# Kernel tuning notes

Hardware: AMD Instinct MI355X
Metric: run time of the kernel (lower is better)

Reference implementation:

```python
import jax, jax.numpy as jnp
import numpy as np
import math

B, S, D, H = 2, 2048, 1024, 16
DK = D // H
EPS = 1e-5

def setup_inputs() -> dict:
    key = jax.random.key(0)
    ks = jax.random.split(key, 16)
    s = 0.02
    return {
        'query': jax.random.normal(ks[0], (B, S, D), jnp.float32),
        'key': jax.random.normal(ks[1], (B, S, D), jnp.float32),
        'value': jax.random.normal(ks[2], (B, S, D), jnp.float32),
        'mask': jax.random.randint(ks[3], (B, 1, S, S), 0, 2, jnp.int32),
        'market_context': jax.random.normal(ks[4], (B, D), jnp.float32),
        'Wq': jax.random.normal(ks[5], (D, D), jnp.float32) * s,
        'bq': jnp.zeros((D,), jnp.float32),
        'Wk': jax.random.normal(ks[6], (D, D), jnp.float32) * s,
        'bk': jnp.zeros((D,), jnp.float32),
        'Wv': jax.random.normal(ks[7], (D, D), jnp.float32) * s,
        'bv': jnp.zeros((D,), jnp.float32),
        'Wo': jax.random.normal(ks[8], (D, D), jnp.float32) * s,
        'bo': jnp.zeros((D,), jnp.float32),
        'Wc': jax.random.normal(ks[9], (D, D), jnp.float32) * s,
        'bc': jnp.zeros((D,), jnp.float32),
        'ln_g': jnp.ones((D,), jnp.float32),
        'ln_b': jnp.zeros((D,), jnp.float32),
    }

def reference(query, key, value, mask, market_context,
              Wq, bq, Wk, bk, Wv, bv, Wo, bo, Wc, bc, ln_g, ln_b):
    b, s, d = query.shape
    # QKV projections -> [B, H, S, DK]
    Q = (query @ Wq + bq).reshape(b, s, H, DK).transpose(0, 2, 1, 3)
    K = (key @ Wk + bk).reshape(b, s, H, DK).transpose(0, 2, 1, 3)
    V = (value @ Wv + bv).reshape(b, s, H, DK).transpose(0, 2, 1, 3)
    # market context -> per-head bias added to K (broadcast over sequence)
    ctx = (market_context @ Wc + bc).reshape(b, H, DK)
    K = K + ctx[:, :, None, :]
    scores = jnp.einsum('bhqd,bhkd->bhqk', Q, K) / math.sqrt(DK)
    scores = jnp.where(mask == 0, jnp.float32(-1e9), scores)
    attn = jax.nn.softmax(scores, axis=-1)  # dropout is identity in eval
    ctx2 = jnp.einsum('bhqk,bhkd->bhqd', attn, V)
    ctx2 = ctx2.transpose(0, 2, 1, 3).reshape(b, s, d)
    out = ctx2 @ Wo + bo
    x = out + query
    mu = jnp.mean(x, axis=-1, keepdims=True)
    var = jnp.mean((x - mu) ** 2, axis=-1, keepdims=True)
    return (x - mu) * jax.lax.rsqrt(var + EPS) * ln_g + ln_b
```

## Files before the change

### kernel.cpp

```cpp
#include <hip/hip_runtime.h>
#include <cstdint>

typedef unsigned short u16;
typedef __attribute__((ext_vector_type(8))) short s16x8;
typedef __attribute__((ext_vector_type(8))) unsigned short u16x8;
typedef __attribute__((ext_vector_type(4))) float f32x4;
typedef __attribute__((ext_vector_type(16))) float f32x16;
typedef __attribute__((ext_vector_type(2))) unsigned uint2v;
typedef __attribute__((ext_vector_type(4))) unsigned uint4v;

#define CKF 0.18033688011f

__device__ inline u16 f2bf(float f){
  union { float f; uint32_t u; } v; v.f = f;
  uint32_t r = v.u + 0x7fffu + ((v.u >> 16) & 1u);
  return (u16)(r >> 16);
}

__device__ inline f32x4 mfma16(s16x8 a, s16x8 b, f32x4 c){
  return __builtin_amdgcn_mfma_f32_16x16x32_bf16(a, b, c, 0, 0, 0);
}
__device__ inline f32x16 mfma32(s16x8 a, s16x8 b, f32x16 c){
  return __builtin_amdgcn_mfma_f32_32x32x16_bf16(a, b, c, 0, 0, 0);
}
__device__ inline unsigned cvtpk(float a, float b){
  unsigned r;
  asm("v_cvt_pk_bf16_f32 %0, %1, %2" : "=v"(r) : "v"(a), "v"(b));
  return r;
}
__device__ inline float exp2a(float x){
  float r;
  asm("v_exp_f32 %0, %1" : "=v"(r) : "v"(x));
  return r;
}
__device__ inline void glds16(const u16* g, u16* l){
  __builtin_amdgcn_global_load_lds((const __attribute__((address_space(1))) void*)g,
                                   (__attribute__((address_space(3))) void*)l, 16, 0, 0);
}
__device__ inline void glds4(const unsigned* g, unsigned* l){
  __builtin_amdgcn_global_load_lds((const __attribute__((address_space(1))) void*)g,
                                   (__attribute__((address_space(3))) void*)l, 4, 0, 0);
}

struct PrepParams {
  const float* q; const float* k; const float* v;
  const int* mask; const float* mc;
  const float* W0; const float* W1; const float* W2; const float* W3;
  const float* Wc;
  u16* qo; u16* ko; u16* vo;
  u16* T0; u16* T1; u16* T2; u16* T3;
  unsigned* bits; float* part;
};

__global__ __launch_bounds__(256) void prep_kernel(PrepParams PP){
  __shared__ float shf[1056];
  int blk = blockIdx.x, tid = threadIdx.x;
  if (blk < 6144){
    int byy = blk >> 11, bxx = blk & 2047;
    const float* src = (byy == 0) ? PP.q : (byy == 1) ? PP.k : PP.v;
    u16* dst = (byy == 0) ? PP.qo : (byy == 1) ? PP.ko : PP.vo;
    size_t i = ((size_t)bxx * 256 + tid) * 8;
    float4 a = *(const float4*)(src + i);
    float4 b = *(const float4*)(src + i + 4);
    u16x8 o = { f2bf(a.x), f2bf(a.y), f2bf(a.z), f2bf(a.w),
                f2bf(b.x), f2bf(b.y), f2bf(b.z), f2bf(b.w) };
    *(u16x8*)(dst + i) = o;
  } else if (blk < 10240){
    int idx = blk - 6144;
    int bxx = idx & 31, byy = (idx >> 5) & 31, bzz = idx >> 10;
    const float* W = (bzz == 0) ? PP.W0 : (bzz == 1) ? PP.W1 : (bzz == 2) ? PP.W2 : PP.W3;
    u16* T = (bzz == 0) ? PP.T0 : (bzz == 1) ? PP.T1 : (bzz == 2) ? PP.T2 : PP.T3;
    float (*t)[33] = (float(*)[33])shf;
    int n0 = bxx * 32, k0 = byy * 32;
    int tx = tid & 31, ty = tid >> 5;
    #pragma unroll
    for (int j = 0; j < 4; j++)
      t[ty + j*8][tx] = W[(size_t)(k0 + ty + j*8) * 1024 + n0 + tx];
    __syncthreads();
    #pragma unroll
    for (int j = 0; j < 4; j++)
      T[(size_t)(n0 + ty + j*8) * 1024 + k0 + tx] = f2bf(t[tx][ty + j*8]);
  } else if (blk < 43008){
    size_t i = (size_t)(blk - 10240) * 256 + tid;
    int v = PP.mask[i];
    unsigned long long bal = __ballot(v != 0);
    int lane = tid & 63;
    if (lane == 0)       PP.bits[i >> 5] = (unsigned)bal;
    else if (lane == 32) PP.bits[i >> 5] = (unsigned)(bal >> 32);
  } else {
    int slice = blk - 43008;
    int k0 = slice * 64;
    float4 a0 = {0.f,0.f,0.f,0.f}, a1 = {0.f,0.f,0.f,0.f};
    const float* wp = PP.Wc + (size_t)k0 * 1024 + tid * 4;
    #pragma unroll 8
    for (int k = 0; k < 64; k++){
      float4 wv = *(const float4*)(wp + (size_t)k * 1024);
      float m0 = PP.mc[k0 + k], m1 = PP.mc[1024 + k0 + k];
      a0.x += m0 * wv.x; a0.y += m0 * wv.y; a0.z += m0 * wv.z; a0.w += m0 * wv.w;
      a1.x += m1 * wv.x; a1.y += m1 * wv.y; a1.z += m1 * wv.z; a1.w += m1 * wv.w;
    }
    *(float4*)(PP.part + ((size_t)slice * 2 + 0) * 1024 + tid * 4) = a0;
    *(float4*)(PP.part + ((size_t)slice * 2 + 1) * 1024 + tid * 4) = a1;
  }
}

__global__ __launch_bounds__(256) void ctxred_kernel(const float* __restrict__ part,
                                                     const float* __restrict__ bc,
                                                     float* __restrict__ ctx){
  int b = blockIdx.x, tid = threadIdx.x;
  float4 s = *(const float4*)(bc + tid * 4);
  #pragma unroll 4
  for (int sl = 0; sl < 16; sl++){
    float4 p = *(const float4*)(part + ((size_t)sl * 2 + b) * 1024 + tid * 4);
    s.x += p.x; s.y += p.y; s.z += p.z; s.w += p.w;
  }
  *(float4*)(ctx + (size_t)b * 1024 + tid * 4) = s;
}

struct GemmParams {
  const u16* A0; const u16* A1; const u16* A2; const u16* A3;
  const u16* W0; const u16* W1; const u16* W2; const u16* W3;
  const float* b0; const float* b1; const float* b2;
  const float* ctx;
  u16* outQ; u16* outK; u16* outV; float* outX0; float* outX1;
  int which;
};

__global__ __launch_bounds__(256) void gemm_kernel(GemmParams P){
  int o = blockIdx.x + (blockIdx.y << 3) + (blockIdx.z << 8);
  int xcd = o & 7, j = o >> 3;
  int by = xcd + ((j & 3) << 3);
  int bx = (j >> 2) & 7;
  int bz = j >> 5;

  int z, kbase, nkt;
  const u16* A; const u16* W;
  if (P.which < 0){
    z = bz; kbase = 0; nkt = 32;
    if (z == 0){ A = P.A0; W = P.W0; }
    else if (z == 1){ A = P.A1; W = P.W1; }
    else { A = P.A2; W = P.W2; }
  } else {
    z = 3; kbase = bz * 512; nkt = 16;
    A = P.A3; W = P.W3;
  }
  int m0 = by * 128, n0 = bx * 128;
  __shared__ __align__(16) u16 sm[24576];
  int tid = threadIdx.x, lane = tid & 63, w = tid >> 6;
  int li = lane & 15, lq = lane >> 4;
  int wm = w >> 1, wn = w & 1;
  f32x4 zero = {0.f, 0.f, 0.f, 0.f};
  f32x4 acc[4][4];
  #pragma unroll
  for (int i = 0; i < 4; i++)
    #pragma unroll
    for (int jj = 0; jj < 4; jj++) acc[i][jj] = zero;

  int scolS = ((lane & 3) ^ ((lane >> 3) & 3)) << 3;
  int row0 = w * 16 + (lane >> 2);
  const u16* aS0 = A + (size_t)(m0 + row0) * 1024 + kbase + scolS;
  const u16* aS1 = aS0 + (size_t)64 * 1024;
  const u16* bS0 = W + (size_t)(n0 + row0) * 1024 + kbase + scolS;
  const u16* bS1 = bS0 + (size_t)64 * 1024;
  int aD0 = (w * 64) * 8, aD1 = (256 + w * 64) * 8;

  int aOff[4], bOff[4];
  #pragma unroll
  for (int mb = 0; mb < 4; mb++){
    int row = wm * 64 + mb * 16 + li;
    aOff[mb] = (row * 32 + ((lq ^ ((row >> 1) & 3)) << 3)) * 2;
  }
  #pragma unroll
  for (int nb = 0; nb < 4; nb++){
    int row = wn * 64 + nb * 16 + li;
    bOff[nb] = 8192 + (row * 32 + ((lq ^ ((row >> 1) & 3)) << 3)) * 2;
  }

  auto STAGE = [&](int ct){
    u16* Ab = &sm[ct * 8192];
    u16* Bb = &sm[ct * 8192 + 4096];
    glds16(aS0, Ab + aD0);
    glds16(aS1, Ab + aD1);
    glds16(bS0, Bb + aD0);
    glds16(bS1, Bb + aD1);
    aS0 += 32; aS1 += 32; bS0 += 32; bS1 += 32;
  };

  auto KITER = [&](int kt, int ct, int cn){
    if (kt + 1 < nkt){
      STAGE(cn);
      asm volatile("s_waitcnt vmcnt(4)" ::: "memory");
    } else {
      asm volatile("s_waitcnt vmcnt(0)" ::: "memory");
    }
    __builtin_amdgcn_sched_barrier(0);
    __builtin_amdgcn_s_barrier();
    const char* base = (const char*)sm + ct * 16384;
    s16x8 af[4], bfr[4];
    #pragma unroll
    for (int mb = 0; mb < 4; mb++) af[mb] = *(const s16x8*)(base + aOff[mb]);
    #pragma unroll
    for (int nb = 0; nb < 4; nb++) bfr[nb] = *(const s16x8*)(base + bOff[nb]);
    __builtin_amdgcn_s_setprio(1);
    #pragma unroll
    for (int mb = 0; mb < 4; mb++)
      #pragma unroll
      for (int nb = 0; nb < 4; nb++)
        acc[mb][nb] = mfma16(af[mb], bfr[nb], acc[mb][nb]);
    __builtin_amdgcn_s_setprio(0);
  };

  STAGE(0);
  if (nkt == 32){
    for (int kt = 0; kt < 30; kt += 3){
      KITER(kt, 0, 1); KITER(kt + 1, 1, 2); KITER(kt + 2, 2, 0);
    }
    KITER(30, 0, 1); KITER(31, 1, 2);
  } else {
    for (int kt = 0; kt < 15; kt += 3){
      KITER(kt, 0, 1); KITER(kt + 1, 1, 2); KITER(kt + 2, 2, 0);
    }
    KITER(15, 0, 1);
  }

  if (z == 2){
    const float* bias = P.b2;
    __syncthreads();
    u16* Ot = sm;
    #pragma unroll
    for (int mb = 0; mb < 4; mb++){
      #pragma unroll
      for (int nb = 0; nb < 4; nb++){
        int colL = wn * 64 + nb * 16 + li;
        int rowB = wm * 64 + mb * 16 + lq * 4;
        float bcol = bias[n0 + colL];
        unsigned p01 = cvtpk(acc[mb][nb][0] + bcol, acc[mb][nb][1] + bcol);
        unsigned p23 = cvtpk(acc[mb][nb][2] + bcol, acc[mb][nb][3] + bcol);
        int ba = colL * 256 + ((rowB * 2) ^ ((colL & 7) << 4));
        *(unsigned*)((char*)Ot + ba) = p01;
        *(unsigned*)((char*)Ot + ba + 4) = p23;
      }
    }
    __syncthreads();
    int bq_ = m0 >> 11, srow0 = m0 & 2047;
    #pragma unroll
    for (int i = 0; i < 8; i++){
      int u = i * 256 + tid;
      int colL = u >> 4, sc = u & 15;
      int ba = colL * 256 + ((sc * 16) ^ ((colL & 7) << 4));
      u16x8 vv = *(const u16x8*)((char*)Ot + ba);
      *(u16x8*)(P.outV + (((size_t)(bq_ * 1024 + n0 + colL)) << 11) + srow0 + sc * 8) = vv;
    }
    return;
  }

  if (z == 3){
    float* Xo = (kbase == 0) ? P.outX0 : P.outX1;
    #pragma unroll
    for (int mb = 0; mb < 4; mb++){
      #pragma unroll
      for (int nb = 0; nb < 4; nb++){
        int col = n0 + wn * 64 + nb * 16 + li;
        #pragma unroll
        for (int r = 0; r < 4; r++){
          int row = m0 + wm * 64 + mb * 16 + lq * 4 + r;
          Xo[(size_t)row * 1024 + col] = acc[mb][nb][r];
        }
      }
    }
    return;
  }

  const float* bias = (z == 0) ? P.b0 : P.b1;
  #pragma unroll
  for (int mb = 0; mb < 4; mb++){
    #pragma unroll
    for (int nb = 0; nb < 4; nb++){
      int colL = wn * 64 + nb * 16 + li; int col = n0 + colL;
      float bcol = bias[col];
      #pragma unroll
      for (int r = 0; r < 4; r++){
        int row = m0 + wm * 64 + mb * 16 + lq * 4 + r;
        float v = acc[mb][nb][r] + bcol;
        if (z == 0){
          P.outQ[(size_t)row * 1024 + col] = f2bf(v * CKF);
        } else {
          v += P.ctx[(size_t)(row >> 11) * 1024 + col];
          P.outK[(size_t)row * 1024 + col] = f2bf(v);
        }
      }
    }
  }
}

__global__ __launch_bounds__(256) void attn_kernel(
    const u16* __restrict__ Qg, const u16* __restrict__ Kg, const u16* __restrict__ Vtg,
    const unsigned* __restrict__ mbits, u16* __restrict__ ctx2){
  __shared__ __align__(16) u16 arena[26112];
  int tid = threadIdx.x, lane = tid & 63, w = tid >> 6;
  int l31 = lane & 31, hi = lane >> 5;
  int r7 = l31 & 7;
  int orig = blockIdx.x + (blockIdx.y << 4);
  int swz = (orig & 7) * 64 + (orig >> 3);
  int q0 = (swz & 15) * 128, bh = swz >> 4, b = bh >> 4, h = bh & 15;
  int qr = w * 32 + l31;

  s16x8 qf[4];
  {
    const u16* qp = Qg + (size_t)(b * 2048 + q0 + qr) * 1024 + h * 64 + hi * 8;
    #pragma unroll
    for (int ks = 0; ks < 4; ks++)
      qf[ks] = *(const s16x8*)(qp + ks * 16);
  }
  s16x8 onesf;
  #pragma unroll
  for (int e = 0; e < 8; e++) onesf[e] = (short)0x3F80;
  f32x16 ZERO;
  #pragma unroll
  for (int r = 0; r < 16; r++) ZERO[r] = 0.f;

  int scolS = ((lane & 7) ^ (lane >> 3)) << 3;
  int rowS = w * 16 + (lane >> 3);
  const u16* kS0 = Kg + (size_t)(b * 2048 + rowS) * 1024 + h * 64 + scolS;
  const u16* kS1 = kS0 + (size_t)8 * 1024;
  const u16* vS0 = Vtg + (((size_t)(bh * 64 + rowS)) << 11) + scolS;
  const u16* vS1 = vS0 + ((size_t)8 << 11);
  int um = w * 64 + lane;
  const unsigned* mS = mbits + (size_t)(b * 2048 + q0 + (um >> 1)) * 64 + (um & 1);
  int kD0 = w * 1024, kD1 = w * 1024 + 512;

  int koff[2][4], voff[2][4];
  #pragma unroll
  for (int jj = 0; jj < 2; jj++)
    #pragma unroll
    for (int ks = 0; ks < 4; ks++){
      koff[jj][ks] = ((jj * 32 + l31) * 64 + (((ks * 2 + hi) ^ r7) << 3)) * 2;
      voff[jj][ks] = 8192 + ((jj * 32 + l31) * 64 + (((ks * 2 + hi) ^ r7) << 3)) * 2;
    }
  int mB = 49152 + qr * 8;

  auto STAGE = [&](int ct){
    u16* dst = &arena[ct * 8192];
    glds16(kS0, dst + kD0);
    glds16(kS1, dst + kD1);
    glds16(vS0, dst + 4096 + kD0);
    glds16(vS1, dst + 4096 + kD1);
    glds4(mS, (unsigned*)&arena[24576] + ct * 256 + w * 64);
    kS0 += (size_t)64 * 1024; kS1 += (size_t)64 * 1024;
    vS0 += 64; vS1 += 64; mS += 2;
  };

  f32x16 accO[2], accS;
  accO[0] = ZERO; accO[1] = ZERO; accS = ZERO;

  STAGE(0);

  auto ITER = [&](int t, int ct, int cn){
    if (t < 31){
      STAGE(cn);
      asm volatile("s_waitcnt vmcnt(5)" ::: "memory");
    } else {
      asm volatile("s_waitcnt vmcnt(0)" ::: "memory");
    }
    __builtin_amdgcn_sched_barrier(0);
    __builtin_amdgcn_s_barrier();
    const char* base = (const char*)arena + ct * 16384;

    f32x16 S[2];
    __builtin_amdgcn_s_setprio(1);
    #pragma unroll
    for (int jj = 0; jj < 2; jj++){
      S[jj] = ZERO;
      #pragma unroll
      for (int ks = 0; ks < 4; ks++){
        s16x8 kf = *(const s16x8*)(base + koff[jj][ks]);
        S[jj] = mfma32(kf, qf[ks], S[jj]);
      }
    }
    __builtin_amdgcn_s_setprio(0);

    uint2v mw = *(const uint2v*)((const char*)arena + mB + ct * 1024);
    unsigned mh0 = mw[0] >> (hi << 2), mh1 = mw[1] >> (hi << 2);
    #pragma unroll
    for (int jj = 0; jj < 2; jj++){
      unsigned mh = jj ? mh1 : mh0;
      #pragma unroll
      for (int rg = 0; rg < 16; rg++){
        int pos = (rg & 3) + ((rg >> 2) << 3);
        float pv = exp2a(S[jj][rg]);
        S[jj][rg] = ((mh >> pos) & 1u) ? pv : 0.f;
      }
    }

    s16x8 pf[4];
    #pragma unroll
    for (int jj = 0; jj < 2; jj++){
      #pragma unroll
      for (int hs = 0; hs < 2; hs++){
        int rb = hs * 8;
        unsigned A0 = cvtpk(S[jj][rb + 0], S[jj][rb + 1]);
        unsigned A1 = cvtpk(S[jj][rb + 2], S[jj][rb + 3]);
        unsigned B0 = cvtpk(S[jj][rb + 4], S[jj][rb + 5]);
        unsigned B1 = cvtpk(S[jj][rb + 6], S[jj][rb + 7]);
        uint2v r01 = __builtin_amdgcn_permlane32_swap(A0, B0, false, false);
        uint2v r23 = __builtin_amdgcn_permlane32_swap(A1, B1, false, false);
        uint4v uu = { r01[0], r23[0], r01[1], r23[1] };
        pf[jj * 2 + hs] = *(s16x8*)&uu;
      }
    }
    __builtin_amdgcn_s_setprio(1);
    #pragma unroll
    for (int c = 0; c < 4; c++){
      #pragma unroll
      for (int dh = 0; dh < 2; dh++){
        s16x8 vf = *(const s16x8*)(base + voff[dh][c]);
        accO[dh] = mfma32(vf, pf[c], accO[dh]);
      }
      accS = mfma32(onesf, pf[c], accS);
    }
    __builtin_amdgcn_s_setprio(0);
  };

  for (int t = 0; t < 30; t += 3){
    ITER(t, 0, 1); ITER(t + 1, 1, 2); ITER(t + 2, 2, 0);
  }
  ITER(30, 0, 1); ITER(31, 1, 2);

  __syncthreads();
  float lsum = accS[0];
  float inv = 1.f / lsum;
  u16* Ot = arena;
  #pragma unroll
  for (int dh = 0; dh < 2; dh++){
    #pragma unroll
    for (int rg = 0; rg < 16; rg += 2){
      int dk = dh * 32 + (rg & 3) + ((rg >> 2) << 3) + (hi << 2);
      unsigned pk = cvtpk(accO[dh][rg] * inv, accO[dh][rg + 1] * inv);
      *(unsigned*)&Ot[qr * 64 + (((dk >> 3) ^ (qr & 7)) << 3) + (dk & 7)] = pk;
    }
  }
  __syncthreads();
  #pragma unroll
  for (int i = 0; i < 4; i++){
    int u = i * 256 + tid, row = u >> 3, slot = u & 7;
    u16x8 vv = *(const u16x8*)&Ot[row * 64 + ((slot ^ (row & 7)) << 3)];
    *(u16x8*)(ctx2 + (size_t)(b * 2048 + q0 + row) * 1024 + h * 64 + slot * 8) = vv;
  }
}

__global__ __launch_bounds__(256) void ln_kernel(const float* __restrict__ X0,
                                                 const float* __restrict__ X1,
                                                 const float* __restrict__ qres,
                                                 const float* __restrict__ bo,
                                                 const float* __restrict__ g,
                                                 const float* __restrict__ bb,
                                                 float* __restrict__ out){
  size_t row = blockIdx.x;
  int tid = threadIdx.x;
  float4 a = *(const float4*)(X0 + row * 1024 + tid * 4);
  float4 c = *(const float4*)(X1 + row * 1024 + tid * 4);
  float4 q = *(const float4*)(qres + row * 1024 + tid * 4);
  float4 bv = *(const float4*)(bo + tid * 4);
  float4 v;
  v.x = a.x + c.x + q.x + bv.x;
  v.y = a.y + c.y + q.y + bv.y;
  v.z = a.z + c.z + q.z + bv.z;
  v.w = a.w + c.w + q.w + bv.w;
  float s = v.x + v.y + v.z + v.w;
  float s2 = v.x*v.x + v.y*v.y + v.z*v.z + v.w*v.w;
  #pragma unroll
  for (int o = 1; o < 64; o <<= 1){
    s += __shfl_xor(s, o, 64);
    s2 += __shfl_xor(s2, o, 64);
  }
  __shared__ float rs[4], rs2[4];
  int w = tid >> 6;
  if ((tid & 63) == 0){ rs[w] = s; rs2[w] = s2; }
  __syncthreads();
  s = rs[0] + rs[1] + rs[2] + rs[3];
  s2 = rs2[0] + rs2[1] + rs2[2] + rs2[3];
  float mu = s * (1.f / 1024.f);
  float var = s2 * (1.f / 1024.f) - mu * mu;
  float rstd = rsqrtf(var + 1e-5f);
  float4 gg = *(const float4*)(g + tid * 4);
  float4 bt = *(const float4*)(bb + tid * 4);
  float4 o;
  o.x = (v.x - mu) * rstd * gg.x + bt.x;
  o.y = (v.y - mu) * rstd * gg.y + bt.y;
  o.z = (v.z - mu) * rstd * gg.z + bt.z;
  o.w = (v.w - mu) * rstd * gg.w + bt.w;
  *(float4*)(out + row * 1024 + tid * 4) = o;
}

extern "C" void kernel_launch(void* const* d_in, const int* in_sizes, int n_in,
                              void* d_out, int out_size, void* d_ws, size_t ws_size,
                              hipStream_t stream){
  const float* query = (const float*)d_in[0];
  const float* key_  = (const float*)d_in[1];
  const float* value = (const float*)d_in[2];
  const int*   mask  = (const int*)d_in[3];
  const float* mc    = (const float*)d_in[4];
  const float* Wq = (const float*)d_in[5];  const float* bq = (const float*)d_in[6];
  const float* Wk = (const float*)d_in[7];  const float* bk = (const float*)d_in[8];
  const float* Wv = (const float*)d_in[9];  const float* bv = (const float*)d_in[10];
  const float* Wo = (const float*)d_in[11]; const float* bo = (const float*)d_in[12];
  const float* Wc = (const float*)d_in[13]; const float* bc = (const float*)d_in[14];
  const float* lng = (const float*)d_in[15]; const float* lnb = (const float*)d_in[16];
  float* outp = (float*)d_out;
  uint8_t* ws = (uint8_t*)d_ws;
  const size_t MB = (size_t)1 << 20;
  if (ws_size < 58 * MB) return;

  u16* q_bf = (u16*)(ws + 0);
  u16* k_bf = (u16*)(ws + 8 * MB);
  u16* v_bf = (u16*)(ws + 16 * MB);
  float* X0 = (float*)(ws + 8 * MB);
  u16* Qb   = (u16*)(ws + 24 * MB);
  u16* Kb   = (u16*)(ws + 32 * MB);
  float* X1 = (float*)(ws + 32 * MB);
  u16* Vt   = (u16*)(ws + 40 * MB);
  u16* Wqt  = (u16*)(ws + 48 * MB);
  u16* Wkt  = (u16*)(ws + 50 * MB);
  u16* Wvt  = (u16*)(ws + 52 * MB);
  u16* Wot  = (u16*)(ws + 54 * MB);
  unsigned* mbits = (unsigned*)(ws + 56 * MB);
  float* ctxf = (float*)(ws + 57 * MB);
  float* ctxpart = (float*)(ws + 57 * MB + 65536);
  u16* ctx2 = q_bf;

  PrepParams PP;
  PP.q = query; PP.k = key_; PP.v = value; PP.mask = mask; PP.mc = mc;
  PP.W0 = Wq; PP.W1 = Wk; PP.W2 = Wv; PP.W3 = Wo; PP.Wc = Wc;
  PP.qo = q_bf; PP.ko = k_bf; PP.vo = v_bf;
  PP.T0 = Wqt; PP.T1 = Wkt; PP.T2 = Wvt; PP.T3 = Wot;
  PP.bits = mbits; PP.part = ctxpart;
  prep_kernel<<<43024, 256, 0, stream>>>(PP);

  ctxred_kernel<<<2, 256, 0, stream>>>(ctxpart, bc, ctxf);

  GemmParams gp;
  gp.A0 = q_bf; gp.A1 = k_bf; gp.A2 = v_bf; gp.A3 = ctx2;
  gp.W0 = Wqt;  gp.W1 = Wkt;  gp.W2 = Wvt;  gp.W3 = Wot;
  gp.b0 = bq;   gp.b1 = bk;   gp.b2 = bv;
  gp.ctx = ctxf;
  gp.outQ = Qb; gp.outK = Kb; gp.outV = Vt; gp.outX0 = X0; gp.outX1 = X1;
  gp.which = -1;
  gemm_kernel<<<dim3(8, 32, 3), 256, 0, stream>>>(gp);

  attn_kernel<<<dim3(16, 32), 256, 0, stream>>>(Qb, Kb, Vt, mbits, ctx2);

  gp.which = 3;
  gemm_kernel<<<dim3(8, 32, 2), 256, 0, stream>>>(gp);

  ln_kernel<<<4096, 256, 0, stream>>>(X0, X1, query, bo, lng, lnb, outp);
}
```

Baseline: 153.0 us.

## Fold context reduction into K-projection epilogue, store output-proj partials in bf16

Removes the separate ctxred kernel launch: the K-projection GEMM epilogue now sums the 16 context partial slices plus biases per column itself. The split-K output-projection partials X0/X1 are stored as bf16 instead of fp32, which halves that write and read traffic for the layernorm kernel at some cost in precision. The attention loop also issues the mask load before the QK MFMAs and starts the accumulation from zero directly. Each K-GEMM block now redundantly reads the partial sums, and bf16 rounding of the partials adds error.

```diff
diff --git a/kernel.cpp b/kernel.cpp
--- a/kernel.cpp
+++ b/kernel.cpp
@@ -2,6 +2,7 @@
 #include <cstdint>
 
 typedef unsigned short u16;
+typedef __attribute__((ext_vector_type(4))) unsigned short us4;
 typedef __attribute__((ext_vector_type(8))) short s16x8;
 typedef __attribute__((ext_vector_type(8))) unsigned short u16x8;
 typedef __attribute__((ext_vector_type(4))) float f32x4;
@@ -15,6 +16,10 @@
   union { float f; uint32_t u; } v; v.f = f;
   uint32_t r = v.u + 0x7fffu + ((v.u >> 16) & 1u);
   return (u16)(r >> 16);
+}
+__device__ inline float bf2f(u16 x){
+  union { uint32_t u; float f; } v; v.u = ((uint32_t)x) << 16;
+  return v.f;
 }
 
 __device__ inline f32x4 mfma16(s16x8 a, s16x8 b, f32x4 c){
@@ -104,25 +109,12 @@
   }
 }
 
-__global__ __launch_bounds__(256) void ctxred_kernel(const float* __restrict__ part,
-                                                     const float* __restrict__ bc,
-                                                     float* __restrict__ ctx){
-  int b = blockIdx.x, tid = threadIdx.x;
-  float4 s = *(const float4*)(bc + tid * 4);
-  #pragma unroll 4
-  for (int sl = 0; sl < 16; sl++){
-    float4 p = *(const float4*)(part + ((size_t)sl * 2 + b) * 1024 + tid * 4);
-    s.x += p.x; s.y += p.y; s.z += p.z; s.w += p.w;
-  }
-  *(float4*)(ctx + (size_t)b * 1024 + tid * 4) = s;
-}
-
 struct GemmParams {
   const u16* A0; const u16* A1; const u16* A2; const u16* A3;
   const u16* W0; const u16* W1; const u16* W2; const u16* W3;
   const float* b0; const float* b1; const float* b2;
-  const float* ctx;
-  u16* outQ; u16* outK; u16* outV; float* outX0; float* outX1;
+  const float* part;
+  u16* outQ; u16* outK; u16* outV; u16* outX0; u16* outX1;
   int which;
 };
 
@@ -255,7 +247,7 @@
   }
 
   if (z == 3){
-    float* Xo = (kbase == 0) ? P.outX0 : P.outX1;
+    u16* Xo = (kbase == 0) ? P.outX0 : P.outX1;
     #pragma unroll
     for (int mb = 0; mb < 4; mb++){
       #pragma unroll
@@ -264,14 +256,42 @@
         #pragma unroll
         for (int r = 0; r < 4; r++){
           int row = m0 + wm * 64 + mb * 16 + lq * 4 + r;
-          Xo[(size_t)row * 1024 + col] = acc[mb][nb][r];
+          Xo[(size_t)row * 1024 + col] = f2bf(acc[mb][nb][r]);
         }
       }
     }
     return;
   }
 
-  const float* bias = (z == 0) ? P.b0 : P.b1;
+  if (z == 1){
+    const float* bcK = (const float*)P.A3;
+    int bidx = m0 >> 11;
+    float ctxl[4];
+    #pragma unroll
+    for (int nb = 0; nb < 4; nb++){
+      int col = n0 + wn * 64 + nb * 16 + li;
+      float s = P.b1[col] + bcK[col];
+      #pragma unroll 4
+      for (int sl = 0; sl < 16; sl++)
+        s += P.part[((size_t)sl * 2 + bidx) * 1024 + col];
+      ctxl[nb] = s;
+    }
+    #pragma unroll
+    for (int mb = 0; mb < 4; mb++){
+      #pragma unroll
+      for (int nb = 0; nb < 4; nb++){
+        int col = n0 + wn * 64 + nb * 16 + li;
+        #pragma unroll
+        for (int r = 0; r < 4; r++){
+          int row = m0 + wm * 64 + mb * 16 + lq * 4 + r;
+          P.outK[(size_t)row * 1024 + col] = f2bf(acc[mb][nb][r] + ctxl[nb]);
+        }
+      }
+    }
+    return;
+  }
+
+  const float* bias = P.b0;
   #pragma unroll
   for (int mb = 0; mb < 4; mb++){
     #pragma unroll
@@ -281,13 +301,7 @@
       #pragma unroll
       for (int r = 0; r < 4; r++){
         int row = m0 + wm * 64 + mb * 16 + lq * 4 + r;
-        float v = acc[mb][nb][r] + bcol;
-        if (z == 0){
-          P.outQ[(size_t)row * 1024 + col] = f2bf(v * CKF);
-        } else {
-          v += P.ctx[(size_t)(row >> 11) * 1024 + col];
-          P.outK[(size_t)row * 1024 + col] = f2bf(v);
-        }
+        P.outQ[(size_t)row * 1024 + col] = f2bf((acc[mb][nb][r] + bcol) * CKF);
       }
     }
   }
@@ -366,20 +380,22 @@
     __builtin_amdgcn_s_barrier();
     const char* base = (const char*)arena + ct * 16384;
 
+    uint2v mw = *(const uint2v*)((const char*)arena + mB + ct * 1024);
+
     f32x16 S[2];
     __builtin_amdgcn_s_setprio(1);
     #pragma unroll
     for (int jj = 0; jj < 2; jj++){
-      S[jj] = ZERO;
-      #pragma unroll
-      for (int ks = 0; ks < 4; ks++){
+      s16x8 kf0 = *(const s16x8*)(base + koff[jj][0]);
+      S[jj] = mfma32(kf0, qf[0], ZERO);
+      #pragma unroll
+      for (int ks = 1; ks < 4; ks++){
         s16x8 kf = *(const s16x8*)(base + koff[jj][ks]);
         S[jj] = mfma32(kf, qf[ks], S[jj]);
       }
     }
     __builtin_amdgcn_s_setprio(0);
 
-    uint2v mw = *(const uint2v*)((const char*)arena + mB + ct * 1024);
     unsigned mh0 = mw[0] >> (hi << 2), mh1 = mw[1] >> (hi << 2);
     #pragma unroll
     for (int jj = 0; jj < 2; jj++){
@@ -448,8 +464,8 @@
   }
 }
 
-__global__ __launch_bounds__(256) void ln_kernel(const float* __restrict__ X0,
-                                                 const float* __restrict__ X1,
+__global__ __launch_bounds__(256) void ln_kernel(const u16* __restrict__ X0b,
+                                                 const u16* __restrict__ X1b,
                                                  const float* __restrict__ qres,
                                                  const float* __restrict__ bo,
                                                  const float* __restrict__ g,
@@ -457,15 +473,15 @@
                                                  float* __restrict__ out){
   size_t row = blockIdx.x;
   int tid = threadIdx.x;
-  float4 a = *(const float4*)(X0 + row * 1024 + tid * 4);
-  float4 c = *(const float4*)(X1 + row * 1024 + tid * 4);
+  us4 a4 = *(const us4*)(X0b + row * 1024 + tid * 4);
+  us4 c4 = *(const us4*)(X1b + row * 1024 + tid * 4);
   float4 q = *(const float4*)(qres + row * 1024 + tid * 4);
   float4 bv = *(const float4*)(bo + tid * 4);
   float4 v;
-  v.x = a.x + c.x + q.x + bv.x;
-  v.y = a.y + c.y + q.y + bv.y;
-  v.z = a.z + c.z + q.z + bv.z;
-  v.w = a.w + c.w + q.w + bv.w;
+  v.x = bf2f(a4[0]) + bf2f(c4[0]) + q.x + bv.x;
+  v.y = bf2f(a4[1]) + bf2f(c4[1]) + q.y + bv.y;
+  v.z = bf2f(a4[2]) + bf2f(c4[2]) + q.z + bv.z;
+  v.w = bf2f(a4[3]) + bf2f(c4[3]) + q.w + bv.w;
   float s = v.x + v.y + v.z + v.w;
   float s2 = v.x*v.x + v.y*v.y + v.z*v.z + v.w*v.w;
   #pragma unroll
@@ -514,18 +530,17 @@
   u16* q_bf = (u16*)(ws + 0);
   u16* k_bf = (u16*)(ws + 8 * MB);
   u16* v_bf = (u16*)(ws + 16 * MB);
-  float* X0 = (float*)(ws + 8 * MB);
+  u16* X0b  = (u16*)(ws + 8 * MB);
   u16* Qb   = (u16*)(ws + 24 * MB);
   u16* Kb   = (u16*)(ws + 32 * MB);
-  float* X1 = (float*)(ws + 32 * MB);
+  u16* X1b  = (u16*)(ws + 32 * MB);
   u16* Vt   = (u16*)(ws + 40 * MB);
   u16* Wqt  = (u16*)(ws + 48 * MB);
   u16* Wkt  = (u16*)(ws + 50 * MB);
   u16* Wvt  = (u16*)(ws + 52 * MB);
   u16* Wot  = (u16*)(ws + 54 * MB);
   unsigned* mbits = (unsigned*)(ws + 56 * MB);
-  float* ctxf = (float*)(ws + 57 * MB);
-  float* ctxpart = (float*)(ws + 57 * MB + 65536);
+  float* ctxpart = (float*)(ws + 57 * MB);
   u16* ctx2 = q_bf;
 
   PrepParams PP;
@@ -536,21 +551,20 @@
   PP.bits = mbits; PP.part = ctxpart;
   prep_kernel<<<43024, 256, 0, stream>>>(PP);
 
-  ctxred_kernel<<<2, 256, 0, stream>>>(ctxpart, bc, ctxf);
-
   GemmParams gp;
-  gp.A0 = q_bf; gp.A1 = k_bf; gp.A2 = v_bf; gp.A3 = ctx2;
+  gp.A0 = q_bf; gp.A1 = k_bf; gp.A2 = v_bf; gp.A3 = (const u16*)bc;
   gp.W0 = Wqt;  gp.W1 = Wkt;  gp.W2 = Wvt;  gp.W3 = Wot;
   gp.b0 = bq;   gp.b1 = bk;   gp.b2 = bv;
-  gp.ctx = ctxf;
-  gp.outQ = Qb; gp.outK = Kb; gp.outV = Vt; gp.outX0 = X0; gp.outX1 = X1;
+  gp.part = ctxpart;
+  gp.outQ = Qb; gp.outK = Kb; gp.outV = Vt; gp.outX0 = X0b; gp.outX1 = X1b;
   gp.which = -1;
   gemm_kernel<<<dim3(8, 32, 3), 256, 0, stream>>>(gp);
 
   attn_kernel<<<dim3(16, 32), 256, 0, stream>>>(Qb, Kb, Vt, mbits, ctx2);
 
+  gp.A3 = ctx2;
   gp.which = 3;
   gemm_kernel<<<dim3(8, 32, 2), 256, 0, stream>>>(gp);
 
-  ln_kernel<<<4096, 256, 0, stream>>>(X0, X1, query, bo, lng, lnb, outp);
-}
+  ln_kernel<<<4096, 256, 0, stream>>>(X0b, X1b, query, bo, lng, lnb, outp);
+}
```

Result: faster. 146.3 us (median of 3 runs) (-4.4%).
